# Performance work log

Measured on AMD Instinct MI355X. Metric: run time of the kernel, lower is better.

## Reference

```python
import jax, jax.numpy as jnp
import numpy as np

N_HEAD = 16
MAX_SEQ_LEN = 2048
RATIO = 1
NEG_INF = -jnp.inf


def make_alibi_bias(n_head: int, max_seq_len: int, ratio: int) -> jnp.ndarray:
    # bias[t, s] = s*ratio - t, masked to -inf where > 0 (future positions)
    s = jnp.arange(max_seq_len)[None, :] * ratio            # [1, S]
    t = jnp.arange(max_seq_len * ratio)[:, None]            # [T, 1]
    bias = (s - t).astype(jnp.float32)                      # [T, S]
    bias = jnp.where(bias > 0, NEG_INF, bias)
    # per-head slopes: cumprod of 2^(-8/n_head) -> m_i = 2^(-8*(i+1)/n_head)
    m = jnp.cumprod(jnp.full((n_head,), 2.0 ** (-8.0 / n_head), dtype=jnp.float32))
    return bias[None, :, :] * m[:, None, None]              # [H, T, S]


def setup_inputs() -> dict:
    key = jax.random.key(0)
    kq, kk, kv = jax.random.split(key, 3)
    B, T, D = 2, 2048, 1024
    return {
        "q": jax.random.normal(kq, (B, T, D), dtype=jnp.float32),
        "k": jax.random.normal(kk, (B, T, D), dtype=jnp.float32),
        "v": jax.random.normal(kv, (B, T, D), dtype=jnp.float32),
    }


def reference(q, k, v):
    B, T, D = q.shape
    S = k.shape[1]
    H = N_HEAD
    dh = D // H
    # split heads: [B, T, D] -> [B, H, T, dh]
    qh = q.reshape(B, T, H, dh).transpose(0, 2, 1, 3)
    kh = k.reshape(B, S, H, dh).transpose(0, 2, 1, 3)
    vh = v.reshape(B, S, H, dh).transpose(0, 2, 1, 3)

    scores = jnp.einsum("bhtd,bhsd->bhts", qh, kh) / jnp.sqrt(jnp.float32(dh))
    bias = make_alibi_bias(H, MAX_SEQ_LEN, RATIO)[:, -T:, -S:]  # [H, T, S]
    attn = jax.nn.softmax(scores + bias[None], axis=-1)
    out = jnp.einsum("bhts,bhsd->bhtd", attn, vh)
    # gather heads: [B, H, T, dh] -> [B, T, D]
    return out.transpose(0, 2, 1, 3).reshape(B, T, D)
```

## Files before the change

kernel.cpp:

```cpp
#include <hip/hip_runtime.h>

#define N_HEAD 16
#define DHEAD 64
#define TSEQ 2048
#define DMODEL 1024
#define BATCH 2

typedef _Float16 f16x8 __attribute__((ext_vector_type(8)));
typedef _Float16 f16x4 __attribute__((ext_vector_type(4)));
typedef _Float16 f16x2 __attribute__((ext_vector_type(2)));
typedef __fp16 fp16x2 __attribute__((ext_vector_type(2)));
typedef float f32x4 __attribute__((ext_vector_type(4)));

union F8 { f16x8 v; uint4 u; f16x2 h[4]; };
union F4 { f16x4 v; uint2 u; f16x2 h[2]; };

#if __has_builtin(__builtin_amdgcn_exp2f)
#define EXP2F(x) __builtin_amdgcn_exp2f(x)
#else
#define EXP2F(x) exp2f(x)
#endif

__device__ __forceinline__ void gload_lds16(const void* g, void* l) {
    __builtin_amdgcn_global_load_lds(
        (const __attribute__((address_space(1))) void*)g,
        (__attribute__((address_space(3))) void*)l, 16, 0, 0);
}

__device__ __forceinline__ f16x2 pk(float a, float b) {
    union { fp16x2 i; f16x2 o; } c;
    c.i = __builtin_amdgcn_cvt_pkrtz(a, b);
    return c.o;
}

__device__ __forceinline__ F8 pack8_f32(const float* p) {
    const float4 a = *(const float4*)p;
    const float4 b = *(const float4*)(p + 4);
    F8 r;
    r.h[0] = pk(a.x, a.y); r.h[1] = pk(a.z, a.w);
    r.h[2] = pk(b.x, b.y); r.h[3] = pk(b.z, b.w);
    return r;
}

__global__ __launch_bounds__(256) void prep(const float* __restrict__ K,
                                            const float* __restrict__ V,
                                            _Float16* __restrict__ Kh,
                                            _Float16* __restrict__ Vh)
{
    __shared__ float tl[64][67];
    const int bh = blockIdx.y, b = bh >> 4, h = bh & 15;
    const int s0 = blockIdx.x * 64;
    const int t = threadIdx.x;
    const int r16 = t >> 4, c4 = (t & 15) * 4;
    #pragma unroll
    for (int pass = 0; pass < 4; ++pass) {
        const int row = pass * 16 + r16;
        const size_t goff = ((size_t)(b * TSEQ + s0 + row)) * DMODEL + h * DHEAD + c4;
        const float4 fk = *(const float4*)(K + goff);
        F4 ok;
        ok.h[0] = pk(fk.x, fk.y);
        ok.h[1] = pk(fk.z, fk.w);
        *(uint2*)(Kh + (((size_t)bh * TSEQ + s0 + row) << 6) + c4) = ok.u;
        const float4 fv = *(const float4*)(V + goff);
        tl[row][c4 + 0] = fv.x; tl[row][c4 + 1] = fv.y;
        tl[row][c4 + 2] = fv.z; tl[row][c4 + 3] = fv.w;
    }
    __syncthreads();
    const int d = t >> 2, sc = (t & 3) * 16;
    F8 p0, p1;
    #pragma unroll
    for (int j = 0; j < 4; ++j) p0.h[j] = pk(tl[sc + 2 * j][d], tl[sc + 2 * j + 1][d]);
    #pragma unroll
    for (int j = 0; j < 4; ++j) p1.h[j] = pk(tl[sc + 8 + 2 * j][d], tl[sc + 9 + 2 * j][d]);
    _Float16* vo = Vh + ((size_t)bh * DHEAD + d) * TSEQ + s0 + sc;
    *(uint4*)vo = p0.u;
    *(uint4*)(vo + 8) = p1.u;
}

__global__ __launch_bounds__(256, 2) void alibi_attn(
    const float* __restrict__ Q, const _Float16* __restrict__ Kh,
    const _Float16* __restrict__ Vh, float* __restrict__ O)
{
    __shared__ __align__(16) char kbuf[2][8192];
    __shared__ __align__(16) char vbuf[2][8192];

    const int wv   = threadIdx.x >> 6;
    const int lane = threadIdx.x & 63;
    const int quad = lane >> 4;
    const int l16  = lane & 15;

    const int bh = blockIdx.x;
    const int b  = bh >> 4, h = bh & 15;
    const int py = blockIdx.y;
    const int qt = (py < 8) ? (15 - py) : (py - 8);
    const int sx2 = 2 * qt + 1;

    const float LOG2E   = 1.44269504088896f;
    const float slope   = exp2f(-0.5f * (float)(h + 1));
    const float bslope2 = slope * LOG2E;
    const float sscale2 = 0.125f * LOG2E;
    const float step64  = 64.0f * bslope2;
    const float rb1 = bslope2, rb2 = 2.f * bslope2, rb3 = 3.f * bslope2;

    const float* qp  = Q + (size_t)b * TSEQ * DMODEL + (size_t)h * DHEAD;
    const char*  kpb = (const char*)(Kh + (size_t)bh * TSEQ * DHEAD);
    const char*  vpb = (const char*)(Vh + (size_t)bh * DHEAD * TSEQ);

    const int st_r  = lane >> 3;
    const int k_src = st_r * 128  + (((lane & 7) ^ st_r) * 16);
    const int v_src = st_r * 4096 + (((lane & 7) ^ st_r) * 16);

    const int koff0 = l16 * 128 + ((quad ^ (l16 & 7)) * 16);
    const int koff1 = l16 * 128 + (((quad + 4) ^ (l16 & 7)) * 16);
    const int vbase = l16 * 128 + (quad & 1) * 8;
    int vx[4];
    #pragma unroll
    for (int sj = 0; sj < 4; ++sj)
        vx[sj] = ((sj * 2 + (quad >> 1)) ^ (l16 & 7)) * 16;

    const f32x4 zero4 = {0.f, 0.f, 0.f, 0.f};

    const int base0 = qt * 128 + wv * 16;
    const int base1 = base0 + 64;

    auto stage = [&](int t) {
        const char* kg = kpb + (size_t)t * 8192;
        const char* vg = vpb + (size_t)t * 128;
        char* kd = kbuf[t & 1];
        char* vd = vbuf[t & 1];
        #pragma unroll
        for (int c = 0; c < 2; ++c) {
            const int gr = wv * 16 + c * 8;
            gload_lds16(kg + gr * 128 + k_src, kd + gr * 128);
            gload_lds16(vg + gr * 4096 + v_src, vd + gr * 128);
        }
    };

    stage(0);

    const float* qr0 = qp + (size_t)(base0 + l16) * DMODEL + quad * 8;
    const float* qr1 = qp + (size_t)(base1 + l16) * DMODEL + quad * 8;
    const F8 aq00 = pack8_f32(qr0);
    const F8 aq01 = pack8_f32(qr0 + 32);
    const F8 aq10 = pack8_f32(qr1);
    const F8 aq11 = pack8_f32(qr1 + 32);

    f32x4 o0[4], o1[4];
    float lp0 = 0.f, lp1 = 0.f;
    float dbq0[4], dbq1[4];
    #pragma unroll
    for (int nt = 0; nt < 4; ++nt) { o0[nt] = zero4; o1[nt] = zero4; }
    #pragma unroll
    for (int sj = 0; sj < 4; ++sj) {
        dbq0[sj] = (float)(sj * 16 + quad * 4 - base0 - l16) * bslope2;
        dbq1[sj] = (float)(sj * 16 + quad * 4 - base1 - l16) * bslope2;
    }

    __syncthreads();

    for (int t = 0; t <= sx2; ++t) {
        if (t < sx2) stage(t + 1);
        const char* kb = kbuf[t & 1];
        const char* vb = vbuf[t & 1];

        F8 kA[4][2];
        #pragma unroll
        for (int sj = 0; sj < 4; ++sj) {
            kA[sj][0].u = *(const uint4*)(kb + sj * 2048 + koff0);
            kA[sj][1].u = *(const uint4*)(kb + sj * 2048 + koff1);
        }

        const bool run0 = (t < sx2);

        f32x4 sT0[4], sT1[4];
        __builtin_amdgcn_s_setprio(1);
        if (run0) {
            #pragma unroll
            for (int sj = 0; sj < 4; ++sj) {
                f32x4 acc = zero4;
                acc = __builtin_amdgcn_mfma_f32_16x16x32_f16(kA[sj][0].v, aq00.v, acc, 0, 0, 0);
                acc = __builtin_amdgcn_mfma_f32_16x16x32_f16(kA[sj][1].v, aq01.v, acc, 0, 0, 0);
                sT0[sj] = acc;
            }
        }
        #pragma unroll
        for (int sj = 0; sj < 4; ++sj) {
            f32x4 acc = zero4;
            acc = __builtin_amdgcn_mfma_f32_16x16x32_f16(kA[sj][0].v, aq10.v, acc, 0, 0, 0);
            acc = __builtin_amdgcn_mfma_f32_16x16x32_f16(kA[sj][1].v, aq11.v, acc, 0, 0, 0);
            sT1[sj] = acc;
        }
        __builtin_amdgcn_s_setprio(0);

        F4 vf[4][4];
        #pragma unroll
        for (int nt = 0; nt < 4; ++nt)
            #pragma unroll
            for (int sj = 0; sj < 4; ++sj)
                vf[nt][sj].u = *(const uint2*)(vb + nt * 2048 + vbase + vx[sj]);

        if (run0) {
            const bool masked = (t == sx2 - 1);
            F4 pP[4];
            #pragma unroll
            for (int sj = 0; sj < 4; ++sj) {
                const float db = dbq0[sj];
                float p0 = EXP2F(fmaf(sT0[sj][0], sscale2, db));
                float p1 = EXP2F(fmaf(sT0[sj][1], sscale2, db + rb1));
                float p2 = EXP2F(fmaf(sT0[sj][2], sscale2, db + rb2));
                float p3 = EXP2F(fmaf(sT0[sj][3], sscale2, db + rb3));
                if (masked) {
                    const int di = t * 64 + sj * 16 + quad * 4 - base0 - l16;
                    if (di + 0 > 0) p0 = 0.f;
                    if (di + 1 > 0) p1 = 0.f;
                    if (di + 2 > 0) p2 = 0.f;
                    if (di + 3 > 0) p3 = 0.f;
                }
                lp0 += (p0 + p1) + (p2 + p3);
                pP[sj].h[0] = pk(p0, p1);
                pP[sj].h[1] = pk(p2, p3);
                dbq0[sj] = db + step64;
            }
            __builtin_amdgcn_s_setprio(1);
            #pragma unroll
            for (int nt = 0; nt < 4; ++nt)
                #pragma unroll
                for (int sj = 0; sj < 4; ++sj)
                    o0[nt] = __builtin_amdgcn_mfma_f32_16x16x16f16(
                        pP[sj].v, vf[nt][sj].v, o0[nt], 0, 0, 0);
            __builtin_amdgcn_s_setprio(0);
        }

        {
            const bool masked = (t == sx2);
            F4 pP[4];
            #pragma unroll
            for (int sj = 0; sj < 4; ++sj) {
                const float db = dbq1[sj];
                float p0 = EXP2F(fmaf(sT1[sj][0], sscale2, db));
                float p1 = EXP2F(fmaf(sT1[sj][1], sscale2, db + rb1));
                float p2 = EXP2F(fmaf(sT1[sj][2], sscale2, db + rb2));
                float p3 = EXP2F(fmaf(sT1[sj][3], sscale2, db + rb3));
                if (masked) {
                    const int di = t * 64 + sj * 16 + quad * 4 - base1 - l16;
                    if (di + 0 > 0) p0 = 0.f;
                    if (di + 1 > 0) p1 = 0.f;
                    if (di + 2 > 0) p2 = 0.f;
                    if (di + 3 > 0) p3 = 0.f;
                }
                lp1 += (p0 + p1) + (p2 + p3);
                pP[sj].h[0] = pk(p0, p1);
                pP[sj].h[1] = pk(p2, p3);
                dbq1[sj] = db + step64;
            }
            __builtin_amdgcn_s_setprio(1);
            #pragma unroll
            for (int nt = 0; nt < 4; ++nt)
                #pragma unroll
                for (int sj = 0; sj < 4; ++sj)
                    o1[nt] = __builtin_amdgcn_mfma_f32_16x16x16f16(
                        pP[sj].v, vf[nt][sj].v, o1[nt], 0, 0, 0);
            __builtin_amdgcn_s_setprio(0);
        }

        __syncthreads();
    }

    #pragma unroll
    for (int m = 0; m < 2; ++m) {
        const float lpm  = m ? lp1 : lp0;
        const f32x4* om  = m ? o1 : o0;
        const int base_m = m ? base1 : base0;
        float ls = lpm;
        ls += __shfl_xor(ls, 16);
        ls += __shfl_xor(ls, 32);
        float lr[4];
        #pragma unroll
        for (int r = 0; r < 4; ++r)
            lr[r] = __shfl(ls, quad * 4 + r);
        #pragma unroll
        for (int nt = 0; nt < 4; ++nt)
            #pragma unroll
            for (int r = 0; r < 4; ++r) {
                const int trow = base_m + quad * 4 + r;
                O[((size_t)b * TSEQ + trow) * DMODEL + h * DHEAD + nt * 16 + l16] =
                    om[nt][r] / lr[r];
            }
    }
}

extern "C" void kernel_launch(void* const* d_in, const int* in_sizes, int n_in,
                              void* d_out, int out_size, void* d_ws, size_t ws_size,
                              hipStream_t stream) {
    const float* q = (const float*)d_in[0];
    const float* k = (const float*)d_in[1];
    const float* v = (const float*)d_in[2];
    float* out = (float*)d_out;

    _Float16* Kh = (_Float16*)d_ws;
    _Float16* Vh = Kh + (size_t)BATCH * N_HEAD * TSEQ * DHEAD;

    prep<<<dim3(TSEQ / 64, BATCH * N_HEAD), 256, 0, stream>>>(k, v, Kh, Vh);
    alibi_attn<<<dim3(BATCH * N_HEAD, 16), 256, 0, stream>>>(q, Kh, Vh, out);
}
```

Before: 141.4 us.

## Split attention into 64-row query tiles with 128-thread blocks

Each block now handles one 64-row query tile with 2 waves (each wave 2x16 rows interleaved by 32) instead of a 128-row tile with 4 waves, doubling the grid to 32 tiles per head. Each tile's two row groups now share the same causal end, so the run0 branch and the separate per-group masking schedule disappear and both P·V MFMA groups run back to back. Tiles are ordered in a zigzag across blockIdx.y for load balance. This gives more, smaller blocks for better CU fill, but each K/V tile is now staged by only 2 waves and reused across fewer query rows, which increases global/LDS traffic per output.

```diff
diff --git a/kernel.cpp b/kernel.cpp
--- a/kernel.cpp
+++ b/kernel.cpp
@@ -77,7 +77,7 @@
     *(uint4*)(vo + 8) = p1.u;
 }
 
-__global__ __launch_bounds__(256, 2) void alibi_attn(
+__global__ __launch_bounds__(128, 2) void alibi_attn(
     const float* __restrict__ Q, const _Float16* __restrict__ Kh,
     const _Float16* __restrict__ Vh, float* __restrict__ O)
 {
@@ -91,9 +91,9 @@
 
     const int bh = blockIdx.x;
     const int b  = bh >> 4, h = bh & 15;
-    const int py = blockIdx.y;
-    const int qt = (py < 8) ? (15 - py) : (py - 8);
-    const int sx2 = 2 * qt + 1;
+    const int by = blockIdx.y;
+    const int g = by >> 3, j = by & 7;
+    const int sx = (g == 0) ? j : (g == 1) ? (15 - j) : (g == 2) ? (16 + j) : (31 - j);
 
     const float LOG2E   = 1.44269504088896f;
     const float slope   = exp2f(-0.5f * (float)(h + 1));
@@ -120,8 +120,8 @@
 
     const f32x4 zero4 = {0.f, 0.f, 0.f, 0.f};
 
-    const int base0 = qt * 128 + wv * 16;
-    const int base1 = base0 + 64;
+    const int base0 = sx * 64 + wv * 16;
+    const int base1 = base0 + 32;
 
     auto stage = [&](int t) {
         const char* kg = kpb + (size_t)t * 8192;
@@ -129,8 +129,8 @@
         char* kd = kbuf[t & 1];
         char* vd = vbuf[t & 1];
         #pragma unroll
-        for (int c = 0; c < 2; ++c) {
-            const int gr = wv * 16 + c * 8;
+        for (int c = 0; c < 4; ++c) {
+            const int gr = wv * 32 + c * 8;
             gload_lds16(kg + gr * 128 + k_src, kd + gr * 128);
             gload_lds16(vg + gr * 4096 + v_src, vd + gr * 128);
         }
@@ -158,8 +158,8 @@
 
     __syncthreads();
 
-    for (int t = 0; t <= sx2; ++t) {
-        if (t < sx2) stage(t + 1);
+    for (int t = 0; t <= sx; ++t) {
+        if (t < sx) stage(t + 1);
         const char* kb = kbuf[t & 1];
         const char* vb = vbuf[t & 1];
 
@@ -170,18 +170,14 @@
             kA[sj][1].u = *(const uint4*)(kb + sj * 2048 + koff1);
         }
 
-        const bool run0 = (t < sx2);
-
         f32x4 sT0[4], sT1[4];
         __builtin_amdgcn_s_setprio(1);
-        if (run0) {
-            #pragma unroll
-            for (int sj = 0; sj < 4; ++sj) {
-                f32x4 acc = zero4;
-                acc = __builtin_amdgcn_mfma_f32_16x16x32_f16(kA[sj][0].v, aq00.v, acc, 0, 0, 0);
-                acc = __builtin_amdgcn_mfma_f32_16x16x32_f16(kA[sj][1].v, aq01.v, acc, 0, 0, 0);
-                sT0[sj] = acc;
-            }
+        #pragma unroll
+        for (int sj = 0; sj < 4; ++sj) {
+            f32x4 acc = zero4;
+            acc = __builtin_amdgcn_mfma_f32_16x16x32_f16(kA[sj][0].v, aq00.v, acc, 0, 0, 0);
+            acc = __builtin_amdgcn_mfma_f32_16x16x32_f16(kA[sj][1].v, aq01.v, acc, 0, 0, 0);
+            sT0[sj] = acc;
         }
         #pragma unroll
         for (int sj = 0; sj < 4; ++sj) {
@@ -199,69 +195,61 @@
             for (int sj = 0; sj < 4; ++sj)
                 vf[nt][sj].u = *(const uint2*)(vb + nt * 2048 + vbase + vx[sj]);
 
-        if (run0) {
-            const bool masked = (t == sx2 - 1);
-            F4 pP[4];
-            #pragma unroll
-            for (int sj = 0; sj < 4; ++sj) {
-                const float db = dbq0[sj];
-                float p0 = EXP2F(fmaf(sT0[sj][0], sscale2, db));
-                float p1 = EXP2F(fmaf(sT0[sj][1], sscale2, db + rb1));
-                float p2 = EXP2F(fmaf(sT0[sj][2], sscale2, db + rb2));
-                float p3 = EXP2F(fmaf(sT0[sj][3], sscale2, db + rb3));
-                if (masked) {
-                    const int di = t * 64 + sj * 16 + quad * 4 - base0 - l16;
-                    if (di + 0 > 0) p0 = 0.f;
-                    if (di + 1 > 0) p1 = 0.f;
-                    if (di + 2 > 0) p2 = 0.f;
-                    if (di + 3 > 0) p3 = 0.f;
-                }
-                lp0 += (p0 + p1) + (p2 + p3);
-                pP[sj].h[0] = pk(p0, p1);
-                pP[sj].h[1] = pk(p2, p3);
-                dbq0[sj] = db + step64;
+        const bool masked = (t == sx);
+        F4 pP0[4], pP1[4];
+        #pragma unroll
+        for (int sj = 0; sj < 4; ++sj) {
+            const float db = dbq0[sj];
+            float p0 = EXP2F(fmaf(sT0[sj][0], sscale2, db));
+            float p1 = EXP2F(fmaf(sT0[sj][1], sscale2, db + rb1));
+            float p2 = EXP2F(fmaf(sT0[sj][2], sscale2, db + rb2));
+            float p3 = EXP2F(fmaf(sT0[sj][3], sscale2, db + rb3));
+            if (masked) {
+                const int di = t * 64 + sj * 16 + quad * 4 - base0 - l16;
+                if (di + 0 > 0) p0 = 0.f;
+                if (di + 1 > 0) p1 = 0.f;
+                if (di + 2 > 0) p2 = 0.f;
+                if (di + 3 > 0) p3 = 0.f;
             }
-            __builtin_amdgcn_s_setprio(1);
-            #pragma unroll
-            for (int nt = 0; nt < 4; ++nt)
-                #pragma unroll
-                for (int sj = 0; sj < 4; ++sj)
-                    o0[nt] = __builtin_amdgcn_mfma_f32_16x16x16f16(
-                        pP[sj].v, vf[nt][sj].v, o0[nt], 0, 0, 0);
-            __builtin_amdgcn_s_setprio(0);
-        }
-
-        {
-            const bool masked = (t == sx2);
-            F4 pP[4];
-            #pragma unroll
-            for (int sj = 0; sj < 4; ++sj) {
-                const float db = dbq1[sj];
-                float p0 = EXP2F(fmaf(sT1[sj][0], sscale2, db));
-                float p1 = EXP2F(fmaf(sT1[sj][1], sscale2, db + rb1));
-                float p2 = EXP2F(fmaf(sT1[sj][2], sscale2, db + rb2));
-                float p3 = EXP2F(fmaf(sT1[sj][3], sscale2, db + rb3));
-                if (masked) {
-                    const int di = t * 64 + sj * 16 + quad * 4 - base1 - l16;
-                    if (di + 0 > 0) p0 = 0.f;
-                    if (di + 1 > 0) p1 = 0.f;
-                    if (di + 2 > 0) p2 = 0.f;
-                    if (di + 3 > 0) p3 = 0.f;
-                }
-                lp1 += (p0 + p1) + (p2 + p3);
-                pP[sj].h[0] = pk(p0, p1);
-                pP[sj].h[1] = pk(p2, p3);
-                dbq1[sj] = db + step64;
+            lp0 += (p0 + p1) + (p2 + p3);
+            pP0[sj].h[0] = pk(p0, p1);
+            pP0[sj].h[1] = pk(p2, p3);
+            dbq0[sj] = db + step64;
+        }
+        #pragma unroll
+        for (int sj = 0; sj < 4; ++sj) {
+            const float db = dbq1[sj];
+            float p0 = EXP2F(fmaf(sT1[sj][0], sscale2, db));
+            float p1 = EXP2F(fmaf(sT1[sj][1], sscale2, db + rb1));
+            float p2 = EXP2F(fmaf(sT1[sj][2], sscale2, db + rb2));
+            float p3 = EXP2F(fmaf(sT1[sj][3], sscale2, db + rb3));
+            if (masked) {
+                const int di = t * 64 + sj * 16 + quad * 4 - base1 - l16;
+                if (di + 0 > 0) p0 = 0.f;
+                if (di + 1 > 0) p1 = 0.f;
+                if (di + 2 > 0) p2 = 0.f;
+                if (di + 3 > 0) p3 = 0.f;
             }
-            __builtin_amdgcn_s_setprio(1);
-            #pragma unroll
-            for (int nt = 0; nt < 4; ++nt)
-                #pragma unroll
-                for (int sj = 0; sj < 4; ++sj)
-                    o1[nt] = __builtin_amdgcn_mfma_f32_16x16x16f16(
-                        pP[sj].v, vf[nt][sj].v, o1[nt], 0, 0, 0);
-            __builtin_amdgcn_s_setprio(0);
-        }
+            lp1 += (p0 + p1) + (p2 + p3);
+            pP1[sj].h[0] = pk(p0, p1);
+            pP1[sj].h[1] = pk(p2, p3);
+            dbq1[sj] = db + step64;
+        }
+
+        __builtin_amdgcn_s_setprio(1);
+        #pragma unroll
+        for (int nt = 0; nt < 4; ++nt)
+            #pragma unroll
+            for (int sj = 0; sj < 4; ++sj)
+                o0[nt] = __builtin_amdgcn_mfma_f32_16x16x16f16(
+                    pP0[sj].v, vf[nt][sj].v, o0[nt], 0, 0, 0);
+        #pragma unroll
+        for (int nt = 0; nt < 4; ++nt)
+            #pragma unroll
+            for (int sj = 0; sj < 4; ++sj)
+                o1[nt] = __builtin_amdgcn_mfma_f32_16x16x16f16(
+                    pP1[sj].v, vf[nt][sj].v, o1[nt], 0, 0, 0);
+        __builtin_amdgcn_s_setprio(0);
 
         __syncthreads();
     }
@@ -301,5 +289,5 @@
     _Float16* Vh = Kh + (size_t)BATCH * N_HEAD * TSEQ * DHEAD;
 
     prep<<<dim3(TSEQ / 64, BATCH * N_HEAD), 256, 0, stream>>>(k, v, Kh, Vh);
-    alibi_attn<<<dim3(BATCH * N_HEAD, 16), 256, 0, stream>>>(q, Kh, Vh, out);
-}
+    alibi_attn<<<dim3(BATCH * N_HEAD, 32), 128, 0, stream>>>(q, Kh, Vh, out);
+}
```

After: 137.1 us. 3.0% less time.
